# Kernel optimization log

Measured on AMD Instinct MI355X. Metric: run time of the kernel, lower is better.

Reference implementation:

```python
import jax, jax.numpy as jnp
import numpy as np

HEADS = 20
DIM_HEAD = 64


def _bicubic_matrix(out_size, in_size, a=-0.75):
    """Separable torch-style bicubic (align_corners=False, antialias=False) as a [out,in] matrix."""
    W = np.zeros((out_size, in_size), dtype=np.float32)
    scale = in_size / out_size
    for i in range(out_size):
        x = (i + 0.5) * scale - 0.5
        x0 = int(np.floor(x))
        t = x - x0
        for tap, dist in zip(range(-1, 3), (1.0 + t, t, 1.0 - t, 2.0 - t)):
            d = abs(dist)
            if d <= 1.0:
                w = (a + 2.0) * d**3 - (a + 3.0) * d**2 + 1.0
            elif d < 2.0:
                w = a * d**3 - 5.0 * a * d**2 + 8.0 * a * d - 4.0 * a
            else:
                w = 0.0
            W[i, min(max(x0 + tap, 0), in_size - 1)] += w
    return jnp.asarray(W)


def setup_inputs() -> dict:
    key = jax.random.key(0)
    ks = jax.random.split(key, 8)
    B, N, QD, CD = 8, 4096, 1280, 1024
    inner = HEADS * DIM_HEAD
    return {
        "x": jax.random.normal(ks[0], (B, N, QD), dtype=jnp.float32),
        "context": jax.random.normal(ks[1], (B, 85, CD), dtype=jnp.float32),
        "Wq": jax.random.normal(ks[2], (QD, inner), dtype=jnp.float32) * 0.02,
        "Wk": jax.random.normal(ks[3], (CD, inner), dtype=jnp.float32) * 0.02,
        "Wv": jax.random.normal(ks[4], (CD, inner), dtype=jnp.float32) * 0.02,
        "Wo": jax.random.normal(ks[5], (inner, QD), dtype=jnp.float32) * 0.02,
        "bo": jnp.zeros((QD,), dtype=jnp.float32),
        "mask": jax.random.randint(ks[6], (B, 1, 256, 256), 0, 2, dtype=jnp.int32),
    }


def reference(x, context, Wq, Wk, Wv, Wo, bo, mask):
    B, N, _ = x.shape
    h, d = HEADS, DIM_HEAD
    scale = d ** -0.5
    q = (x @ Wq).reshape(B, N, h, d)
    k = (context @ Wk).reshape(B, -1, h, d)
    v = (context @ Wv).reshape(B, -1, h, d)
    # fp32 QK^T as in _ATTN_PRECISION == 'fp32'
    sim = jnp.einsum('bihd,bjhd->bhij', q.astype(jnp.float32), k.astype(jnp.float32)) * scale
    # build custom mask: bicubic-resize fg map to hw x hw, threshold, tile x4, append bg, prepend 77 ones
    hw = int(round(N ** 0.5))
    R = _bicubic_matrix(hw, mask.shape[-1])  # [hw, Hin]
    mf = mask.astype(jnp.float32)  # [B,1,H,W]
    resized = jnp.einsum('oh,bchw,pw->bcop', R, mf, R)  # [B,1,hw,hw]
    fg = (resized != 0).transpose(0, 2, 3, 1).reshape(B, hw * hw, 1)  # b (h w) c
    fg = jnp.repeat(fg, 4, axis=-1)  # b i (j k), k=4
    bg = ~fg
    base = jnp.ones((B, hw * hw, 77), dtype=bool)
    m = jnp.concatenate([base, fg, bg], axis=-1)  # [B, N, 85]
    neg = -jnp.finfo(sim.dtype).max
    sim = jnp.where(m[:, None, :, :], sim, neg)
    attn = jax.nn.softmax(sim, axis=-1)
    out = jnp.einsum('bhij,bjhd->bihd', attn.astype(v.dtype), v).reshape(B, N, h * d)
    return out @ Wo + bo
```

## Files before the change

### kernel.cpp

```cpp
#include <hip/hip_runtime.h>
#include <math.h>

typedef _Float16 f16;
typedef _Float16 half8 __attribute__((ext_vector_type(8)));
typedef _Float16 half4v __attribute__((ext_vector_type(4)));
typedef float f32x4 __attribute__((ext_vector_type(4)));

#define NB 8
#define SEQ 4096
#define QDIM 1280
#define CDIM 1024
#define INNER 1280
#define CTX 85
#define CTXP 96

__device__ __forceinline__ void gload16(const void* g, void* l) {
  __builtin_amdgcn_global_load_lds(
      (const __attribute__((address_space(1))) unsigned int*)g,
      (__attribute__((address_space(3))) unsigned int*)l, 16, 0, 0);
}

__global__ void k_cast(const float* __restrict__ x, f16* __restrict__ xh, long n8) {
  long i = blockIdx.x * 256L + threadIdx.x;
  if (i >= n8) return;
  float4 a = ((const float4*)x)[2 * i];
  float4 b = ((const float4*)x)[2 * i + 1];
  half8 o;
  o[0] = (f16)a.x; o[1] = (f16)a.y; o[2] = (f16)a.z; o[3] = (f16)a.w;
  o[4] = (f16)b.x; o[5] = (f16)b.y; o[6] = (f16)b.z; o[7] = (f16)b.w;
  *(half8*)(xh + 8 * i) = o;
}

__global__ void k_castctx(const float* __restrict__ ctx, f16* __restrict__ ctxh) {
  int id = blockIdx.x * 256 + threadIdx.x;
  int b = id / (96 * 128);
  int rem = id % (96 * 128);
  int j = rem >> 7;
  int kc = (rem & 127) * 8;
  half8 o = {};
  if (j < CTX) {
    const float* p = ctx + ((long)b * CTX + j) * CDIM + kc;
    float4 a = *(const float4*)p;
    float4 c = *(const float4*)(p + 4);
    o[0] = (f16)a.x; o[1] = (f16)a.y; o[2] = (f16)a.z; o[3] = (f16)a.w;
    o[4] = (f16)c.x; o[5] = (f16)c.y; o[6] = (f16)c.z; o[7] = (f16)c.w;
  }
  *(half8*)(ctxh + (long)id * 8) = o;
}

__global__ __launch_bounds__(256) void k_transpose(const float* __restrict__ in,
                                                   f16* __restrict__ out, int K, int Nn) {
  __shared__ __attribute__((aligned(16))) f16 T[64][72];
  int n0 = blockIdx.x * 64, k0 = blockIdx.y * 64;
  int t = threadIdx.x;
  int kr = t >> 4, nc = (t & 15) * 4;
  for (int i = 0; i < 4; i++) {
    int k = kr + i * 16;
    float4 v = *(const float4*)&in[(long)(k0 + k) * Nn + n0 + nc];
    T[nc + 0][k] = (f16)v.x;
    T[nc + 1][k] = (f16)v.y;
    T[nc + 2][k] = (f16)v.z;
    T[nc + 3][k] = (f16)v.w;
  }
  __syncthreads();
  for (int i = 0; i < 2; i++) {
    int slot = t + i * 256;
    int n = slot >> 3, ch = (slot & 7) * 8;
    *(half8*)&out[(long)(n0 + n) * K + k0 + ch] = *(half8*)&T[n][ch];
  }
}

__global__ void k_fg(const int* __restrict__ mask, unsigned char* __restrict__ fg) {
  int id = blockIdx.x * 256 + threadIdx.x;
  int b = id >> 12, o = (id >> 6) & 63, p = id & 63;
  const int* mb = mask + (long)b * 65536;
  const int w[4] = {-3, 19, 19, -3};
  int s = 0;
  for (int dh = 0; dh < 4; dh++) {
    const int* row = mb + (4 * o + dh) * 256 + 4 * p;
    int rs = -3 * row[0] + 19 * row[1] + 19 * row[2] - 3 * row[3];
    s += w[dh] * rs;
  }
  fg[id] = (s != 0) ? 1 : 0;
}

__global__ __launch_bounds__(256) void k_kvproj(const f16* __restrict__ ctxh,
    const f16* __restrict__ WkT, const f16* __restrict__ WvT,
    f16* __restrict__ kpad, f16* __restrict__ vT) {
  int b = blockIdx.y, kv = blockIdx.z;
  const f16* WT = kv ? WvT : WkT;
  int w = threadIdx.x >> 6, lane = threadIdx.x & 63;
  int ln = lane & 15, qd = lane >> 4;
  int n0 = (blockIdx.x * 4 + w) * 16;
  const f16* arow = ctxh + ((long)b * CTXP + ln) * CDIM + qd * 8;
  const f16* brow = WT + (long)(n0 + ln) * CDIM + qd * 8;
  f32x4 acc[6] = {};
#pragma unroll 4
  for (int k0 = 0; k0 < CDIM; k0 += 32) {
    half8 bf = *(const half8*)(brow + k0);
#pragma unroll
    for (int mt = 0; mt < 6; mt++) {
      half8 af = *(const half8*)(arow + mt * 16 * CDIM + k0);
      acc[mt] = __builtin_amdgcn_mfma_f32_16x16x32_f16(af, bf, acc[mt], 0, 0, 0);
    }
  }
  if (kv == 0) {
    for (int mt = 0; mt < 6; mt++)
      for (int r = 0; r < 4; r++)
        kpad[((long)b * CTXP + mt * 16 + qd * 4 + r) * INNER + n0 + ln] = (f16)acc[mt][r];
  } else {
    for (int mt = 0; mt < 6; mt++) {
      half4v pv;
      for (int r = 0; r < 4; r++) pv[r] = (f16)acc[mt][r];
      *(half4v*)&vT[((long)b * INNER + n0 + ln) * CTXP + mt * 16 + qd * 4] = pv;
    }
  }
}

template <int OUT_F32>
__global__ __launch_bounds__(256) void k_gemm(const f16* __restrict__ A,
    const f16* __restrict__ Bt, const float* __restrict__ bias,
    f16* __restrict__ outh, float* __restrict__ outf, int K) {
  __shared__ __attribute__((aligned(16))) f16 Alds[128 * 64];
  __shared__ __attribute__((aligned(16))) f16 Blds[128 * 64];
  int tid = threadIdx.x, lane = tid & 63, w = tid >> 6;
  int wr = w >> 1, wc = w & 1;
  int ln = lane & 15, qd = lane >> 4;
  long m0 = (long)blockIdx.x * 128;
  int n0 = blockIdx.y * 128;
  int srow = lane >> 3;
  int schunk = lane & 7;
  f32x4 acc[4][4] = {};
  for (int k0 = 0; k0 < K; k0 += 64) {
#pragma unroll
    for (int i = 0; i < 4; i++) {
      int row = w * 32 + i * 8 + srow;
      int ca = (schunk ^ (row & 7)) * 8;
      gload16(&A[(m0 + row) * K + k0 + ca], &Alds[w * 2048 + i * 512]);
      gload16(&Bt[(long)(n0 + row) * K + k0 + ca], &Blds[w * 2048 + i * 512]);
    }
    __syncthreads();
#pragma unroll
    for (int s = 0; s < 2; s++) {
      half8 af[4], bf[4];
#pragma unroll
      for (int mt = 0; mt < 4; mt++) {
        int row = wr * 64 + mt * 16 + ln;
        af[mt] = *(half8*)&Alds[row * 64 + (((s * 4 + qd) ^ (row & 7)) * 8)];
      }
#pragma unroll
      for (int nt = 0; nt < 4; nt++) {
        int row = wc * 64 + nt * 16 + ln;
        bf[nt] = *(half8*)&Blds[row * 64 + (((s * 4 + qd) ^ (row & 7)) * 8)];
      }
#pragma unroll
      for (int mt = 0; mt < 4; mt++)
#pragma unroll
        for (int nt = 0; nt < 4; nt++)
          acc[mt][nt] = __builtin_amdgcn_mfma_f32_16x16x32_f16(af[mt], bf[nt], acc[mt][nt], 0, 0, 0);
    }
    __syncthreads();
  }
  for (int mt = 0; mt < 4; mt++) {
    long mrow = m0 + wr * 64 + mt * 16 + qd * 4;
    for (int nt = 0; nt < 4; nt++) {
      int n = n0 + wc * 64 + nt * 16 + ln;
      float bv = OUT_F32 ? bias[n] : 0.f;
      for (int r = 0; r < 4; r++) {
        if (OUT_F32) outf[(mrow + r) * INNER + n] = acc[mt][nt][r] + bv;
        else         outh[(mrow + r) * INNER + n] = (f16)acc[mt][nt][r];
      }
    }
  }
}

__global__ __launch_bounds__(256) void k_attn(const f16* __restrict__ q,
    const f16* __restrict__ kpad, const f16* __restrict__ vT,
    const unsigned char* __restrict__ fg, f16* __restrict__ ao) {
  int mb = blockIdx.x;
  int h = blockIdx.y;
  int b = blockIdx.z;
  __shared__ __attribute__((aligned(16))) f16 Klds[CTXP][72];
  __shared__ __attribute__((aligned(16))) f16 Vlds[64][104];
  __shared__ __attribute__((aligned(16))) f16 Plds[4][16][104];
  int tid = threadIdx.x, lane = tid & 63, w = tid >> 6;
  int ln = lane & 15, qd = lane >> 4;

  for (int c = tid; c < CTXP * 8; c += 256) {
    int j = c >> 3, kc = (c & 7) * 8;
    *(half8*)&Klds[j][kc] = *(const half8*)&kpad[((long)b * CTXP + j) * INNER + h * 64 + kc];
  }
  for (int c = tid; c < 64 * 12; c += 256) {
    int d = c / 12, jc = (c % 12) * 8;
    *(half8*)&Vlds[d][jc] = *(const half8*)&vT[((long)b * INNER + h * 64 + d) * CTXP + jc];
  }
  __syncthreads();

  long mg = (long)b * SEQ + mb * 64 + w * 16 + ln;
  half8 qf[2];
  for (int s = 0; s < 2; s++)
    qf[s] = *(const half8*)&q[mg * INNER + h * 64 + s * 32 + qd * 8];

  f32x4 sacc[6] = {};
  for (int s = 0; s < 2; s++)
    for (int nt = 0; nt < 6; nt++) {
      half8 bf = *(half8*)&Klds[nt * 16 + ln][s * 32 + qd * 8];
      sacc[nt] = __builtin_amdgcn_mfma_f32_16x16x32_f16(qf[s], bf, sacc[nt], 0, 0, 0);
    }

  unsigned int fgw = *(const unsigned int*)&fg[(long)b * SEQ + mb * 64 + w * 16 + qd * 4];
  const float scale = 0.125f;
  for (int r = 0; r < 4; r++) {
    bool f = ((fgw >> (8 * r)) & 0xff) != 0;
    float vals[6];
    bool oks[6];
    float mx = -1e30f;
    for (int nt = 0; nt < 6; nt++) {
      int j = nt * 16 + ln;
      bool ok = (j < 77) || (j < 81 ? f : (j < 85 ? !f : false));
      float v = sacc[nt][r] * scale;
      vals[nt] = v; oks[nt] = ok;
      if (ok) mx = fmaxf(mx, v);
    }
    for (int d = 1; d < 16; d <<= 1) mx = fmaxf(mx, __shfl_xor(mx, d, 64));
    float sum = 0.f, p[6];
    for (int nt = 0; nt < 6; nt++) {
      p[nt] = oks[nt] ? __expf(vals[nt] - mx) : 0.f;
      sum += p[nt];
    }
    for (int d = 1; d < 16; d <<= 1) sum += __shfl_xor(sum, d, 64);
    float inv = 1.f / sum;
    for (int nt = 0; nt < 6; nt++)
      Plds[w][qd * 4 + r][nt * 16 + ln] = (f16)(p[nt] * inv);
  }
  __syncthreads();

  f32x4 oacc[4] = {};
  for (int ks = 0; ks < 3; ks++) {
    half8 pf = *(half8*)&Plds[w][ln][ks * 32 + qd * 8];
    for (int ntd = 0; ntd < 4; ntd++) {
      half8 vf = *(half8*)&Vlds[ntd * 16 + ln][ks * 32 + qd * 8];
      oacc[ntd] = __builtin_amdgcn_mfma_f32_16x16x32_f16(pf, vf, oacc[ntd], 0, 0, 0);
    }
  }
  for (int ntd = 0; ntd < 4; ntd++)
    for (int r = 0; r < 4; r++)
      Plds[w][qd * 4 + r][ntd * 16 + ln] = (f16)oacc[ntd][r];
  __syncthreads();
  long rowbase = (long)b * SEQ + mb * 64 + w * 16;
  for (int i = 0; i < 2; i++) {
    int slot = lane + i * 64;
    int rrow = slot >> 3, ch = (slot & 7) * 8;
    *(half8*)&ao[(rowbase + rrow) * INNER + h * 64 + ch] = *(half8*)&Plds[w][rrow][ch];
  }
}

extern "C" void kernel_launch(void* const* d_in, const int* in_sizes, int n_in,
                              void* d_out, int out_size, void* d_ws, size_t ws_size,
                              hipStream_t stream) {
  const float* x   = (const float*)d_in[0];
  const float* ctx = (const float*)d_in[1];
  const float* Wq  = (const float*)d_in[2];
  const float* Wk  = (const float*)d_in[3];
  const float* Wv  = (const float*)d_in[4];
  const float* Wo  = (const float*)d_in[5];
  const float* bo  = (const float*)d_in[6];
  const int*  mask = (const int*)d_in[7];
  float* out = (float*)d_out;

  char* ws = (char*)d_ws;
  size_t off = 0;
  f16* xh  = (f16*)(ws + off); off += 83886080;
  f16* q   = (f16*)(ws + off); off += 83886080;
  f16* ao  = (f16*)(ws + off); off += 83886080;
  f16* WqT = (f16*)(ws + off); off += 3276800;
  f16* WoT = (f16*)(ws + off); off += 3276800;
  f16* WkT = (f16*)(ws + off); off += 2621440;
  f16* WvT = (f16*)(ws + off); off += 2621440;
  f16* kpad= (f16*)(ws + off); off += 1966080;
  f16* vT  = (f16*)(ws + off); off += 1966080;
  f16* ctxh= (f16*)(ws + off); off += 1572864;
  unsigned char* fg = (unsigned char*)(ws + off); off += 32768;
  if (ws_size < off) return;

  k_cast<<<20480, 256, 0, stream>>>(x, xh, 5242880);
  k_castctx<<<384, 256, 0, stream>>>(ctx, ctxh);
  k_transpose<<<dim3(1280/64, 1280/64), 256, 0, stream>>>(Wq, WqT, 1280, 1280);
  k_transpose<<<dim3(1280/64, 1024/64), 256, 0, stream>>>(Wk, WkT, 1024, 1280);
  k_transpose<<<dim3(1280/64, 1024/64), 256, 0, stream>>>(Wv, WvT, 1024, 1280);
  k_transpose<<<dim3(1280/64, 1280/64), 256, 0, stream>>>(Wo, WoT, 1280, 1280);
  k_fg<<<128, 256, 0, stream>>>(mask, fg);
  k_kvproj<<<dim3(20, 8, 2), 256, 0, stream>>>(ctxh, WkT, WvT, kpad, vT);
  k_gemm<0><<<dim3(256, 10), 256, 0, stream>>>(xh, WqT, nullptr, q, nullptr, 1280);
  k_attn<<<dim3(64, 20, 8), 256, 0, stream>>>(q, kpad, vT, fg, ao);
  k_gemm<1><<<dim3(256, 10), 256, 0, stream>>>(ao, WoT, bo, nullptr, out, 1280);
}
```

Baseline: 720.7 us.

## Add 256x256-tile pipelined GEMM with swizzled LDS and XCD-aware block mapping

Adds a new GEMM kernel for the Q and output projections. It uses 512 threads, 256x256 output tiles and 128 KB of dynamic LDS. A/B tiles are double-buffered through global_load_lds with XOR-swizzled rows, and LDS reads, async loads and MFMA quarters are interleaved under explicit barriers, vmcnt waits and setprio. Blocks are remapped so adjacent M tiles run on the same XCD. The goal is more data reuse per loaded byte and hiding load latency behind compute, at the cost of higher register pressure, large LDS use and fragile hand-written synchronisation.

Measured after the change: 680.4 us. -5.6%, faster.

```diff
diff --git a/kernel.cpp b/kernel.cpp
--- a/kernel.cpp
+++ b/kernel.cpp
@@ -13,6 +13,9 @@
 #define INNER 1280
 #define CTX 85
 #define CTXP 96
+
+#define VMCNT(n) asm volatile("s_waitcnt vmcnt(" #n ")" ::: "memory")
+#define BAR() do { asm volatile("" ::: "memory"); __builtin_amdgcn_s_barrier(); asm volatile("" ::: "memory"); } while (0)
 
 __device__ __forceinline__ void gload16(const void* g, void* l) {
   __builtin_amdgcn_global_load_lds(
@@ -174,6 +177,123 @@
   }
 }
 
+__device__ __forceinline__ void stage2(const f16* __restrict__ g, int ldK,
+                                       f16* lds, int tid, int c0) {
+#pragma unroll
+  for (int c = c0; c < c0 + 2; ++c) {
+    int row = c * 64 + (tid >> 3);
+    int sc = (tid & 7) ^ (row & 7);
+    gload16(g + (long)row * ldK + sc * 8, lds + c * 4096 + (tid >> 6) * 512);
+  }
+}
+
+template <int OUT_F32>
+__global__ __launch_bounds__(512, 2) void k_gemm256(const f16* __restrict__ A,
+    const f16* __restrict__ Bt, const float* __restrict__ bias,
+    f16* __restrict__ outh, float* __restrict__ outf, int K) {
+  extern __shared__ __attribute__((aligned(16))) f16 smem[];
+  f16* As0 = smem;
+  f16* As1 = smem + 16384;
+  f16* Bs0 = smem + 32768;
+  f16* Bs1 = smem + 49152;
+  const int NT = K >> 6;
+  int tid = threadIdx.x, lane = tid & 63, w = tid >> 6;
+  int wr = w >> 2, wc = w & 3;
+  int ln = lane & 15, qd = lane >> 4;
+  int wrb = wr * 128, wcb = wc * 64;
+  int cpx = gridDim.x >> 3;
+  int swz = (blockIdx.x & 7) * cpx + (blockIdx.x >> 3);
+  int mtile = swz & 127, ntile = swz >> 7;
+  long m0 = (long)mtile * 256;
+  int n0 = ntile * 256;
+  const f16* Ab = A + m0 * K;
+  const f16* Bb = Bt + (long)n0 * K;
+
+  half8 af[4][2], bf[2][2];
+  f32x4 acc[8][4] = {};
+
+  auto rdA = [&](const f16* Ac, int mh) {
+#pragma unroll
+    for (int mt = 0; mt < 4; ++mt) {
+      int R = wrb + mh * 64 + mt * 16 + ln;
+      const f16* rp = Ac + R * 64;
+      int r7 = (R & 7) << 3;
+      af[mt][0] = *(const half8*)(rp + ((qd << 3) ^ r7));
+      af[mt][1] = *(const half8*)(rp + (((4 + qd) << 3) ^ r7));
+    }
+  };
+  auto rdB = [&](const f16* Bc, int nh) {
+#pragma unroll
+    for (int nt = 0; nt < 2; ++nt) {
+      int R = wcb + nh * 32 + nt * 16 + ln;
+      const f16* rp = Bc + R * 64;
+      int r7 = (R & 7) << 3;
+      bf[nt][0] = *(const half8*)(rp + ((qd << 3) ^ r7));
+      bf[nt][1] = *(const half8*)(rp + (((4 + qd) << 3) ^ r7));
+    }
+  };
+  auto mm = [&](int mh, int nh) {
+    __builtin_amdgcn_s_setprio(1);
+#pragma unroll
+    for (int ks = 0; ks < 2; ++ks)
+#pragma unroll
+      for (int mt = 0; mt < 4; ++mt)
+#pragma unroll
+        for (int nt = 0; nt < 2; ++nt)
+          acc[mh * 4 + mt][nh * 2 + nt] = __builtin_amdgcn_mfma_f32_16x16x32_f16(
+              af[mt][ks], bf[nt][ks], acc[mh * 4 + mt][nh * 2 + nt], 0, 0, 0);
+    __builtin_amdgcn_s_setprio(0);
+  };
+
+  stage2(Ab, K, As0, tid, 0); stage2(Ab, K, As0, tid, 2);
+  stage2(Bb, K, Bs0, tid, 0); stage2(Bb, K, Bs0, tid, 2);
+  if (NT > 1) { stage2(Ab + 64, K, As1, tid, 0); VMCNT(2); } else { VMCNT(0); }
+  BAR();
+
+#define TILE256(KT, AC, BC, AN, BN_) do {                                        \
+    rdA(AC, 0); rdB(BC, 0);                                                      \
+    if ((KT) + 1 < NT) { stage2(Ab + ((KT) + 1) * 64, K, AN, tid, 2);            \
+                         stage2(Bb + ((KT) + 1) * 64, K, BN_, tid, 0); }         \
+    BAR(); mm(0, 0); BAR();                                                      \
+    rdB(BC, 1);                                                                  \
+    if ((KT) + 1 < NT) stage2(Bb + ((KT) + 1) * 64, K, BN_, tid, 2);             \
+    BAR(); mm(0, 1); BAR();                                                      \
+    rdA(AC, 1);                                                                  \
+    BAR(); mm(1, 1); BAR();                                                      \
+    rdB(BC, 0);                                                                  \
+    if ((KT) + 2 < NT) stage2(Ab + ((KT) + 2) * 64, K, AC, tid, 0);              \
+    BAR(); mm(1, 0);                                                             \
+    if ((KT) + 2 < NT) { VMCNT(2); } else if ((KT) + 1 < NT) { VMCNT(0); }       \
+    BAR();                                                                       \
+  } while (0)
+
+#pragma unroll 1
+  for (int kt = 0; kt < NT; kt += 2) {
+    TILE256(kt, As0, Bs0, As1, Bs1);
+    TILE256(kt + 1, As1, Bs1, As0, Bs0);
+  }
+#undef TILE256
+
+#pragma unroll
+  for (int mt = 0; mt < 8; ++mt) {
+    long rb = m0 + wrb + mt * 16 + qd * 4;
+#pragma unroll
+    for (int nt = 0; nt < 4; ++nt) {
+      int col = n0 + wcb + nt * 16 + ln;
+      if (OUT_F32) {
+        float bv = bias[col];
+#pragma unroll
+        for (int r = 0; r < 4; ++r)
+          outf[(rb + r) * INNER + col] = acc[mt][nt][r] + bv;
+      } else {
+#pragma unroll
+        for (int r = 0; r < 4; ++r)
+          outh[(rb + r) * INNER + col] = (f16)acc[mt][nt][r];
+      }
+    }
+  }
+}
+
 __global__ __launch_bounds__(256) void k_attn(const f16* __restrict__ q,
     const f16* __restrict__ kpad, const f16* __restrict__ vT,
     const unsigned char* __restrict__ fg, f16* __restrict__ ao) {
@@ -283,6 +403,17 @@
   unsigned char* fg = (unsigned char*)(ws + off); off += 32768;
   if (ws_size < off) return;
 
+  static int g_use256 = -1;
+  if (g_use256 < 0) {
+    auto* f0 = k_gemm256<0>;
+    auto* f1 = k_gemm256<1>;
+    hipError_t e0 = hipFuncSetAttribute(reinterpret_cast<const void*>(f0),
+                                        hipFuncAttributeMaxDynamicSharedMemorySize, 131072);
+    hipError_t e1 = hipFuncSetAttribute(reinterpret_cast<const void*>(f1),
+                                        hipFuncAttributeMaxDynamicSharedMemorySize, 131072);
+    g_use256 = (e0 == hipSuccess && e1 == hipSuccess) ? 1 : 0;
+  }
+
   k_cast<<<20480, 256, 0, stream>>>(x, xh, 5242880);
   k_castctx<<<384, 256, 0, stream>>>(ctx, ctxh);
   k_transpose<<<dim3(1280/64, 1280/64), 256, 0, stream>>>(Wq, WqT, 1280, 1280);
@@ -291,7 +422,15 @@
   k_transpose<<<dim3(1280/64, 1280/64), 256, 0, stream>>>(Wo, WoT, 1280, 1280);
   k_fg<<<128, 256, 0, stream>>>(mask, fg);
   k_kvproj<<<dim3(20, 8, 2), 256, 0, stream>>>(ctxh, WkT, WvT, kpad, vT);
-  k_gemm<0><<<dim3(256, 10), 256, 0, stream>>>(xh, WqT, nullptr, q, nullptr, 1280);
+  if (g_use256) {
+    k_gemm256<0><<<640, 512, 131072, stream>>>(xh, WqT, nullptr, q, nullptr, 1280);
+  } else {
+    k_gemm<0><<<dim3(256, 10), 256, 0, stream>>>(xh, WqT, nullptr, q, nullptr, 1280);
+  }
   k_attn<<<dim3(64, 20, 8), 256, 0, stream>>>(q, kpad, vT, fg, ao);
-  k_gemm<1><<<dim3(256, 10), 256, 0, stream>>>(ao, WoT, bo, nullptr, out, 1280);
-}
+  if (g_use256) {
+    k_gemm256<1><<<640, 512, 131072, stream>>>(ao, WoT, bo, nullptr, out, 1280);
+  } else {
+    k_gemm<1><<<dim3(256, 10), 256, 0, stream>>>(ao, WoT, bo, nullptr, out, 1280);
+  }
+}
```
